# Kernel tuning notes

Measured on AMD Instinct MI355X. Metric: run time of the kernel, lower is better.

Reference implementation:

```python
import jax, jax.numpy as jnp
import numpy as np

EMBED_DIM = 1024
NUM_HEADS = 16
HEAD_DIM = EMBED_DIM // NUM_HEADS
B, S = 2, 2048


def setup_inputs() -> dict:
    key = jax.random.key(0)
    ks = jax.random.split(key, 10)
    inp = {
        "query": jax.random.normal(ks[0], (B, S, EMBED_DIM), dtype=jnp.float32),
        "key": jax.random.normal(ks[1], (B, S, EMBED_DIM), dtype=jnp.float32),
        "value": jax.random.normal(ks[2], (B, S, EMBED_DIM), dtype=jnp.float32),
        # 0 => masked key position (matches attn_mask == 0 in the torch code)
        "attn_mask": jax.random.randint(ks[3], (B, S), 0, 2, dtype=jnp.int32),
        "Wq": jax.random.normal(ks[4], (EMBED_DIM, EMBED_DIM), dtype=jnp.float32) * 0.02,
        "bq": jnp.zeros((EMBED_DIM,), dtype=jnp.float32),
        "Wk": jax.random.normal(ks[5], (EMBED_DIM, EMBED_DIM), dtype=jnp.float32) * 0.02,
        "bk": jnp.zeros((EMBED_DIM,), dtype=jnp.float32),
        "Wv": jax.random.normal(ks[6], (EMBED_DIM, EMBED_DIM), dtype=jnp.float32) * 0.02,
        "bv": jnp.zeros((EMBED_DIM,), dtype=jnp.float32),
    }
    return inp


def _proj_heads(x, W, b):
    # x: [B, S, E] -> [B, H, S, D]  (nn.Linear uses x @ W.T + b)
    y = x @ W.T + b
    Bx, Sx, E = y.shape
    return y.reshape(Bx, Sx, NUM_HEADS, HEAD_DIM).transpose(0, 2, 1, 3)


def reference(query, key, value, attn_mask, Wq, bq, Wk, bk, Wv, bv):
    q = _proj_heads(query, Wq, bq)   # [B,H,S,D]
    k = _proj_heads(key, Wk, bk)     # [B,H,S,D]
    v = _proj_heads(value, Wv, bv)   # [B,H,S,D]
    inv_scale = float(EMBED_DIM) ** 0.5  # NOTE: original divides by sqrt(embed_dim), not sqrt(head_dim)
    scores = jnp.einsum("bhqd,bhkd->bhqk", q, k) / inv_scale  # [B,H,S,S]
    mask = (attn_mask == 0)[:, None, None, :]  # [B,1,1,S] -> broadcast over [B,H,S,S]
    scores = jnp.where(mask, -jnp.inf, scores)
    attn = jax.nn.softmax(scores, axis=-1)
    # dropout omitted for deterministic reference (see notes)
    out = jnp.einsum("bhqk,bhkd->bhqd", attn, v)  # [B,H,S,D]
    return out
```

## Files before the change

kernel.cpp:

```cpp
#include <hip/hip_runtime.h>
#include <hip/hip_bf16.h>

constexpr int BB = 2;
constexpr int SS = 2048;
constexpr int EE = 1024;
constexpr int HH = 16;
constexpr int DD = 64;
constexpr int MM = BB * SS;
constexpr int CX = MM * EE;
constexpr int CW = EE * EE;
#define QSCALE 0.045084220027780106f
#define NEGBIG -1e30f

typedef __attribute__((ext_vector_type(8))) short short8;
typedef __attribute__((ext_vector_type(4))) float floatx4;

__device__ inline short bf16bits(float x) {
    __hip_bfloat16 h = __float2bfloat16(x);
    return *reinterpret_cast<short*>(&h);
}

__device__ inline unsigned pkbf(float a, float b) {
    return (unsigned)(unsigned short)bf16bits(a) |
           ((unsigned)(unsigned short)bf16bits(b) << 16);
}

__device__ inline float fast_exp2(float x) {
#if __has_builtin(__builtin_amdgcn_exp2f)
    return __builtin_amdgcn_exp2f(x);
#else
    return exp2f(x);
#endif
}

__device__ inline void gl_lds16(const __hip_bfloat16* g, short* l) {
    __builtin_amdgcn_global_load_lds(
        (const __attribute__((address_space(1))) void*)g,
        (__attribute__((address_space(3))) void*)l, 16, 0, 0);
}

__global__ __launch_bounds__(256) void convert_kernel(
    const float* __restrict__ x0, const float* __restrict__ x1, const float* __restrict__ x2,
    const float* __restrict__ w0, const float* __restrict__ w1, const float* __restrict__ w2,
    __hip_bfloat16* __restrict__ xb, __hip_bfloat16* __restrict__ wb)
{
    const int z = blockIdx.z;
    const float* src;
    __hip_bfloat16* dst;
    int count;
    if (z < 3) {
        src = (z == 0) ? x0 : (z == 1) ? x1 : x2;
        dst = xb + (size_t)z * CX;
        count = CX;
    } else {
        src = (z == 3) ? w0 : (z == 4) ? w1 : w2;
        dst = wb + (size_t)(z - 3) * CW;
        count = CW;
    }
    const int idx = (blockIdx.x * 256 + threadIdx.x) * 8;
    if (idx >= count) return;
    const float4 a = reinterpret_cast<const float4*>(src + idx)[0];
    const float4 b = reinterpret_cast<const float4*>(src + idx)[1];
    short8 r;
    r[0] = bf16bits(a.x); r[1] = bf16bits(a.y); r[2] = bf16bits(a.z); r[3] = bf16bits(a.w);
    r[4] = bf16bits(b.x); r[5] = bf16bits(b.y); r[6] = bf16bits(b.z); r[7] = bf16bits(b.w);
    *reinterpret_cast<short8*>(dst + idx) = r;
}

__global__ __launch_bounds__(256) void maskbias_kernel(
    const int* __restrict__ am, float* __restrict__ mb)
{
    const int i = blockIdx.x * 256 + threadIdx.x;
    if (i < BB * SS) mb[i] = (am[i] != 0) ? 0.f : NEGBIG;
}

__global__ __launch_bounds__(256) void proj_gemm(
    const __hip_bfloat16* __restrict__ xb,
    const __hip_bfloat16* __restrict__ wb,
    const float* __restrict__ bq, const float* __restrict__ bk, const float* __restrict__ bv,
    __hip_bfloat16* __restrict__ qws,
    __hip_bfloat16* __restrict__ kws,
    __hip_bfloat16* __restrict__ vtws)
{
    const int which = blockIdx.z;
    const __hip_bfloat16* A = xb + (size_t)which * CX;
    const __hip_bfloat16* W = wb + (size_t)which * CW;
    const float* bias = (which == 0) ? bq : (which == 1) ? bk : bv;

    const int m0   = blockIdx.x * 128;
    const int n0   = blockIdx.y * 128;
    const int tid  = threadIdx.x;
    const int wave = tid >> 6;
    const int lane = tid & 63;
    const int l15  = lane & 15;
    const int quad = lane >> 4;
    const int wr   = wave >> 1;
    const int wc   = wave & 1;

    __shared__ __align__(16) short As[128 * 32];
    __shared__ __align__(16) short Bs[128 * 32];

    const int lrow = (lane >> 2);
    const int lk   = (lane & 3) * 8;

    floatx4 acc[4][4] = {};

    for (int k0 = 0; k0 < EE; k0 += 32) {
        __syncthreads();
        #pragma unroll
        for (int i = 0; i < 2; ++i) {
            gl_lds16(A + (size_t)(m0 + i * 64 + wave * 16 + lrow) * EE + k0 + lk,
                     As + (i * 64 + wave * 16) * 32);
            gl_lds16(W + (size_t)(n0 + i * 64 + wave * 16 + lrow) * EE + k0 + lk,
                     Bs + (i * 64 + wave * 16) * 32);
        }
        __syncthreads();

        short8 af[4], bf[4];
        #pragma unroll
        for (int mt = 0; mt < 4; ++mt)
            af[mt] = *reinterpret_cast<const short8*>(As + (wr * 64 + mt * 16 + l15) * 32 + quad * 8);
        #pragma unroll
        for (int nt = 0; nt < 4; ++nt)
            bf[nt] = *reinterpret_cast<const short8*>(Bs + (wc * 64 + nt * 16 + l15) * 32 + quad * 8);

        #pragma unroll
        for (int mt = 0; mt < 4; ++mt)
            #pragma unroll
            for (int nt = 0; nt < 4; ++nt)
                acc[mt][nt] = __builtin_amdgcn_mfma_f32_16x16x32_bf16(af[mt], bf[nt], acc[mt][nt], 0, 0, 0);
    }

    #pragma unroll
    for (int nt = 0; nt < 4; ++nt) {
        const int n = n0 + wc * 64 + nt * 16 + l15;
        const float bval = bias[n];
        const int h = n >> 6, d = n & 63;
        #pragma unroll
        for (int mt = 0; mt < 4; ++mt) {
            #pragma unroll
            for (int r = 0; r < 4; ++r) {
                const int m = m0 + wr * 64 + mt * 16 + quad * 4 + r;
                const int b = m >> 11;
                const int s = m & (SS - 1);
                float val = acc[mt][nt][r] + bval;
                if (which == 0) val *= QSCALE;
                const __hip_bfloat16 hv = __float2bfloat16(val);
                if (which == 0)
                    qws[(((size_t)b * HH + h) * SS + s) * DD + d] = hv;
                else if (which == 1)
                    kws[(((size_t)b * HH + h) * SS + s) * DD + d] = hv;
                else
                    vtws[(((size_t)b * HH + h) * DD + d) * SS + s] = hv;
            }
        }
    }
}

__global__ __launch_bounds__(256) void attn_kernel(
    const __hip_bfloat16* __restrict__ qws,
    const __hip_bfloat16* __restrict__ kws,
    const __hip_bfloat16* __restrict__ vtws,
    const float* __restrict__ maskbias,
    float* __restrict__ out)
{
    const int bh   = blockIdx.y;
    const int b    = bh >> 4;
    const int q0   = blockIdx.x * 64;
    const int tid  = threadIdx.x;
    const int wave = tid >> 6;
    const int lane = tid & 63;
    const int l15  = lane & 15;
    const int quad = lane >> 4;

    const __hip_bfloat16* Q  = qws  + (size_t)bh * SS * DD;
    const __hip_bfloat16* K  = kws  + (size_t)bh * SS * DD;
    const __hip_bfloat16* VT = vtws + (size_t)bh * DD * SS;
    const float* mb = maskbias + b * SS;

    __shared__ __align__(16) short Ks[64 * 72];
    __shared__ __align__(16) short Vs[64 * 72];
    __shared__ __align__(16) short Ps[4][16 * 72];
    short* pw = Ps[wave];

    const int qrow = q0 + wave * 16 + l15;
    const short8 qa0 = *reinterpret_cast<const short8*>(Q + (size_t)qrow * DD + quad * 8);
    const short8 qa1 = *reinterpret_cast<const short8*>(Q + (size_t)qrow * DD + 32 + quad * 8);

    float m_run = NEGBIG, l_run = 0.f;
    floatx4 acc[4] = {};

    for (int kt = 0; kt < SS; kt += 64) {
        __syncthreads();

        #pragma unroll
        for (int p = 0; p < 2; ++p) {
            const int flat = tid + p * 256;
            const int row = flat >> 3;
            const int g   = flat & 7;
            *reinterpret_cast<short8*>(Ks + row * 72 + g * 8) =
                *reinterpret_cast<const short8*>(K + (size_t)(kt + row) * DD + g * 8);
            *reinterpret_cast<short8*>(Vs + row * 72 + g * 8) =
                *reinterpret_cast<const short8*>(VT + (size_t)row * SS + kt + g * 8);
        }
        __syncthreads();

        floatx4 st[4];
        #pragma unroll
        for (int f = 0; f < 4; ++f) {
            const short8 ka = *reinterpret_cast<const short8*>(Ks + (f * 16 + l15) * 72 + quad * 8);
            const short8 kb = *reinterpret_cast<const short8*>(Ks + (f * 16 + l15) * 72 + 32 + quad * 8);
            floatx4 z = {};
            z = __builtin_amdgcn_mfma_f32_16x16x32_bf16(ka, qa0, z, 0, 0, 0);
            z = __builtin_amdgcn_mfma_f32_16x16x32_bf16(kb, qa1, z, 0, 0, 0);
            st[f] = z;
        }

        #pragma unroll
        for (int f = 0; f < 4; ++f) {
            const float4 m4 = *reinterpret_cast<const float4*>(mb + kt + f * 16 + quad * 4);
            st[f][0] += m4.x; st[f][1] += m4.y; st[f][2] += m4.z; st[f][3] += m4.w;
        }

        float mx = st[0][0];
        #pragma unroll
        for (int f = 0; f < 4; ++f)
            #pragma unroll
            for (int r = 0; r < 4; ++r)
                mx = fmaxf(mx, st[f][r]);
        mx = fmaxf(mx, __shfl_xor(mx, 16, 64));
        mx = fmaxf(mx, __shfl_xor(mx, 32, 64));

        const float mnew = fmaxf(m_run, mx);
        const float alpha = fast_exp2(m_run - mnew);
        m_run = mnew;

        float psum = 0.f;
        #pragma unroll
        for (int f = 0; f < 4; ++f)
            #pragma unroll
            for (int r = 0; r < 4; ++r) {
                const float p = fast_exp2(st[f][r] - mnew);
                st[f][r] = p;
                psum += p;
            }
        psum += __shfl_xor(psum, 16, 64);
        psum += __shfl_xor(psum, 32, 64);
        l_run = l_run * alpha + psum;

        #pragma unroll
        for (int f = 0; f < 4; ++f) {
            *reinterpret_cast<unsigned*>(pw + l15 * 72 + f * 16 + quad * 4) =
                pkbf(st[f][0], st[f][1]);
            *reinterpret_cast<unsigned*>(pw + l15 * 72 + f * 16 + quad * 4 + 2) =
                pkbf(st[f][2], st[f][3]);
        }
        __asm__ volatile("s_waitcnt lgkmcnt(0)" ::: "memory");

        const short8 pa0 = *reinterpret_cast<const short8*>(pw + l15 * 72 + quad * 8);
        const short8 pa1 = *reinterpret_cast<const short8*>(pw + l15 * 72 + 32 + quad * 8);

        float alphaq[4];
        #pragma unroll
        for (int r = 0; r < 4; ++r)
            alphaq[r] = __shfl(alpha, quad * 4 + r, 16);
        #pragma unroll
        for (int nt = 0; nt < 4; ++nt)
            #pragma unroll
            for (int r = 0; r < 4; ++r)
                acc[nt][r] *= alphaq[r];

        #pragma unroll
        for (int nt = 0; nt < 4; ++nt) {
            const short8 vb0 = *reinterpret_cast<const short8*>(Vs + (nt * 16 + l15) * 72 + quad * 8);
            const short8 vb1 = *reinterpret_cast<const short8*>(Vs + (nt * 16 + l15) * 72 + 32 + quad * 8);
            acc[nt] = __builtin_amdgcn_mfma_f32_16x16x32_bf16(pa0, vb0, acc[nt], 0, 0, 0);
            acc[nt] = __builtin_amdgcn_mfma_f32_16x16x32_bf16(pa1, vb1, acc[nt], 0, 0, 0);
        }
    }

    float lq[4];
    #pragma unroll
    for (int r = 0; r < 4; ++r)
        lq[r] = __shfl(l_run, quad * 4 + r, 16);
    const size_t obase = (size_t)bh * SS * DD;
    #pragma unroll
    for (int nt = 0; nt < 4; ++nt)
        #pragma unroll
        for (int r = 0; r < 4; ++r) {
            const int qq = q0 + wave * 16 + quad * 4 + r;
            const int d  = nt * 16 + l15;
            out[obase + (size_t)qq * DD + d] = acc[nt][r] / lq[r];
        }
}

extern "C" void kernel_launch(void* const* d_in, const int* in_sizes, int n_in,
                              void* d_out, int out_size, void* d_ws, size_t ws_size,
                              hipStream_t stream) {
    const float* q    = (const float*)d_in[0];
    const float* k    = (const float*)d_in[1];
    const float* v    = (const float*)d_in[2];
    const int*   mask = (const int*)d_in[3];
    const float* Wq   = (const float*)d_in[4];
    const float* bq   = (const float*)d_in[5];
    const float* Wk   = (const float*)d_in[6];
    const float* bk   = (const float*)d_in[7];
    const float* Wv   = (const float*)d_in[8];
    const float* bv   = (const float*)d_in[9];
    float* out = (float*)d_out;

    __hip_bfloat16* qws  = (__hip_bfloat16*)d_ws;
    __hip_bfloat16* kws  = qws + (size_t)CX;
    __hip_bfloat16* vtws = kws + (size_t)CX;
    __hip_bfloat16* xb   = vtws + (size_t)CX;
    __hip_bfloat16* wb   = xb + (size_t)3 * CX;
    float* mbias = (float*)(wb + (size_t)3 * CW);

    convert_kernel<<<dim3(CX / (256 * 8), 1, 6), 256, 0, stream>>>(
        q, k, v, Wq, Wk, Wv, xb, wb);
    maskbias_kernel<<<dim3((BB * SS) / 256), 256, 0, stream>>>(mask, mbias);
    proj_gemm<<<dim3(MM / 128, EE / 128, 3), 256, 0, stream>>>(
        xb, wb, bq, bk, bv, qws, kws, vtws);
    attn_kernel<<<dim3(SS / 64, BB * HH), 256, 0, stream>>>(
        qws, kws, vtws, mbias, out);
}
```

Measured before the change: 235.3 us.

## Double-buffer LDS tiles with async global-to-LDS loads and XOR-swizzled layouts

The projection GEMM and the attention kernel now use double-buffered LDS tiles. The next K-tile is issued with global_load_lds before the current one is consumed, which lets each iteration drop to a single barrier and overlap global loads with MFMA work. The attention kernel also replaces its padded K/V/P layouts (stride 72) with unpadded rows and an XOR swizzle, so K and V can be DMA'd straight into LDS without bank conflicts. The convert kernel now runs on a flat 1D grid sized to the real element count instead of launching idle blocks for the smaller weight tensors. The cost is twice the LDS per block and a correctness dependence on the async loads being complete at the single barrier.

```diff
diff --git a/kernel.cpp b/kernel.cpp
--- a/kernel.cpp
+++ b/kernel.cpp
@@ -33,7 +33,7 @@
 #endif
 }
 
-__device__ inline void gl_lds16(const __hip_bfloat16* g, short* l) {
+__device__ inline void gl_lds16(const __hip_bfloat16* g, const short* l) {
     __builtin_amdgcn_global_load_lds(
         (const __attribute__((address_space(1))) void*)g,
         (__attribute__((address_space(3))) void*)l, 16, 0, 0);
@@ -44,27 +44,27 @@
     const float* __restrict__ w0, const float* __restrict__ w1, const float* __restrict__ w2,
     __hip_bfloat16* __restrict__ xb, __hip_bfloat16* __restrict__ wb)
 {
-    const int z = blockIdx.z;
+    const long long e = (long long)(blockIdx.x * 256 + threadIdx.x) * 8;
     const float* src;
     __hip_bfloat16* dst;
-    int count;
-    if (z < 3) {
-        src = (z == 0) ? x0 : (z == 1) ? x1 : x2;
-        dst = xb + (size_t)z * CX;
-        count = CX;
+    if (e < 3LL * CX) {
+        const int z = (int)(e >> 22);
+        const int off = (int)(e & (CX - 1));
+        src = ((z == 0) ? x0 : (z == 1) ? x1 : x2) + off;
+        dst = xb + e;
     } else {
-        src = (z == 3) ? w0 : (z == 4) ? w1 : w2;
-        dst = wb + (size_t)(z - 3) * CW;
-        count = CW;
+        const long long e2 = e - 3LL * CX;
+        const int z = (int)(e2 >> 20);
+        const int off = (int)(e2 & (CW - 1));
+        src = ((z == 0) ? w0 : (z == 1) ? w1 : w2) + off;
+        dst = wb + e2;
     }
-    const int idx = (blockIdx.x * 256 + threadIdx.x) * 8;
-    if (idx >= count) return;
-    const float4 a = reinterpret_cast<const float4*>(src + idx)[0];
-    const float4 b = reinterpret_cast<const float4*>(src + idx)[1];
+    const float4 a = reinterpret_cast<const float4*>(src)[0];
+    const float4 b = reinterpret_cast<const float4*>(src)[1];
     short8 r;
     r[0] = bf16bits(a.x); r[1] = bf16bits(a.y); r[2] = bf16bits(a.z); r[3] = bf16bits(a.w);
     r[4] = bf16bits(b.x); r[5] = bf16bits(b.y); r[6] = bf16bits(b.z); r[7] = bf16bits(b.w);
-    *reinterpret_cast<short8*>(dst + idx) = r;
+    *reinterpret_cast<short8*>(dst) = r;
 }
 
 __global__ __launch_bounds__(256) void maskbias_kernel(
@@ -97,32 +97,37 @@
     const int wr   = wave >> 1;
     const int wc   = wave & 1;
 
-    __shared__ __align__(16) short As[128 * 32];
-    __shared__ __align__(16) short Bs[128 * 32];
-
-    const int lrow = (lane >> 2);
+    __shared__ __align__(16) short As[2][128 * 32];
+    __shared__ __align__(16) short Bs[2][128 * 32];
+
+    const int lrow = lane >> 2;
     const int lk   = (lane & 3) * 8;
 
     floatx4 acc[4][4] = {};
 
-    for (int k0 = 0; k0 < EE; k0 += 32) {
+    auto issue = [&](int k0, int buf) {
+        #pragma unroll
+        for (int i = 0; i < 2; ++i) {
+            const int row = i * 64 + wave * 16;
+            gl_lds16(A + (size_t)(m0 + row + lrow) * EE + k0 + lk, &As[buf][row * 32]);
+            gl_lds16(W + (size_t)(n0 + row + lrow) * EE + k0 + lk, &Bs[buf][row * 32]);
+        }
+    };
+
+    issue(0, 0);
+
+    for (int t = 0; t < EE / 32; ++t) {
+        const int buf = t & 1;
         __syncthreads();
-        #pragma unroll
-        for (int i = 0; i < 2; ++i) {
-            gl_lds16(A + (size_t)(m0 + i * 64 + wave * 16 + lrow) * EE + k0 + lk,
-                     As + (i * 64 + wave * 16) * 32);
-            gl_lds16(W + (size_t)(n0 + i * 64 + wave * 16 + lrow) * EE + k0 + lk,
-                     Bs + (i * 64 + wave * 16) * 32);
-        }
-        __syncthreads();
+        if (t + 1 < EE / 32) issue((t + 1) * 32, buf ^ 1);
 
         short8 af[4], bf[4];
         #pragma unroll
         for (int mt = 0; mt < 4; ++mt)
-            af[mt] = *reinterpret_cast<const short8*>(As + (wr * 64 + mt * 16 + l15) * 32 + quad * 8);
+            af[mt] = *reinterpret_cast<const short8*>(&As[buf][(wr * 64 + mt * 16 + l15) * 32 + quad * 8]);
         #pragma unroll
         for (int nt = 0; nt < 4; ++nt)
-            bf[nt] = *reinterpret_cast<const short8*>(Bs + (wc * 64 + nt * 16 + l15) * 32 + quad * 8);
+            bf[nt] = *reinterpret_cast<const short8*>(&Bs[buf][(wc * 64 + nt * 16 + l15) * 32 + quad * 8]);
 
         #pragma unroll
         for (int mt = 0; mt < 4; ++mt)
@@ -178,38 +183,46 @@
     const __hip_bfloat16* VT = vtws + (size_t)bh * DD * SS;
     const float* mb = maskbias + b * SS;
 
-    __shared__ __align__(16) short Ks[64 * 72];
-    __shared__ __align__(16) short Vs[64 * 72];
-    __shared__ __align__(16) short Ps[4][16 * 72];
+    __shared__ __align__(16) short Ks[2][64 * 64];
+    __shared__ __align__(16) short Vs[2][64 * 64];
+    __shared__ __align__(16) short Ps[4][16 * 64];
     short* pw = Ps[wave];
 
     const int qrow = q0 + wave * 16 + l15;
     const short8 qa0 = *reinterpret_cast<const short8*>(Q + (size_t)qrow * DD + quad * 8);
     const short8 qa1 = *reinterpret_cast<const short8*>(Q + (size_t)qrow * DD + 32 + quad * 8);
 
+    const int srow = lane >> 3;
+    const int sg   = ((lane & 7) ^ srow) * 8;
+
+    auto issue = [&](int kt, int buf) {
+        #pragma unroll
+        for (int p = 0; p < 2; ++p) {
+            const int rb = wave * 16 + p * 8;
+            gl_lds16(K + (size_t)(kt + rb + srow) * DD + sg, &Ks[buf][rb * 64]);
+            gl_lds16(VT + (size_t)(rb + srow) * SS + kt + sg, &Vs[buf][rb * 64]);
+        }
+    };
+
+    const int swz = (l15 & 7);
+
     float m_run = NEGBIG, l_run = 0.f;
     floatx4 acc[4] = {};
 
-    for (int kt = 0; kt < SS; kt += 64) {
+    issue(0, 0);
+
+    for (int t = 0; t < SS / 64; ++t) {
+        const int buf = t & 1;
+        const int kt = t * 64;
         __syncthreads();
-
-        #pragma unroll
-        for (int p = 0; p < 2; ++p) {
-            const int flat = tid + p * 256;
-            const int row = flat >> 3;
-            const int g   = flat & 7;
-            *reinterpret_cast<short8*>(Ks + row * 72 + g * 8) =
-                *reinterpret_cast<const short8*>(K + (size_t)(kt + row) * DD + g * 8);
-            *reinterpret_cast<short8*>(Vs + row * 72 + g * 8) =
-                *reinterpret_cast<const short8*>(VT + (size_t)row * SS + kt + g * 8);
-        }
-        __syncthreads();
+        if (t + 1 < SS / 64) issue(kt + 64, buf ^ 1);
 
         floatx4 st[4];
         #pragma unroll
         for (int f = 0; f < 4; ++f) {
-            const short8 ka = *reinterpret_cast<const short8*>(Ks + (f * 16 + l15) * 72 + quad * 8);
-            const short8 kb = *reinterpret_cast<const short8*>(Ks + (f * 16 + l15) * 72 + 32 + quad * 8);
+            const int krow = (f * 16 + l15) * 64;
+            const short8 ka = *reinterpret_cast<const short8*>(&Ks[buf][krow + (quad ^ swz) * 8]);
+            const short8 kb = *reinterpret_cast<const short8*>(&Ks[buf][krow + ((quad + 4) ^ swz) * 8]);
             floatx4 z = {};
             z = __builtin_amdgcn_mfma_f32_16x16x32_bf16(ka, qa0, z, 0, 0, 0);
             z = __builtin_amdgcn_mfma_f32_16x16x32_bf16(kb, qa1, z, 0, 0, 0);
@@ -250,15 +263,16 @@
 
         #pragma unroll
         for (int f = 0; f < 4; ++f) {
-            *reinterpret_cast<unsigned*>(pw + l15 * 72 + f * 16 + quad * 4) =
-                pkbf(st[f][0], st[f][1]);
-            *reinterpret_cast<unsigned*>(pw + l15 * 72 + f * 16 + quad * 4 + 2) =
-                pkbf(st[f][2], st[f][3]);
+            const int g0 = (2 * f + (quad >> 1)) ^ swz;
+            uint2 pk;
+            pk.x = pkbf(st[f][0], st[f][1]);
+            pk.y = pkbf(st[f][2], st[f][3]);
+            *reinterpret_cast<uint2*>(pw + l15 * 64 + g0 * 8 + (quad & 1) * 4) = pk;
         }
         __asm__ volatile("s_waitcnt lgkmcnt(0)" ::: "memory");
 
-        const short8 pa0 = *reinterpret_cast<const short8*>(pw + l15 * 72 + quad * 8);
-        const short8 pa1 = *reinterpret_cast<const short8*>(pw + l15 * 72 + 32 + quad * 8);
+        const short8 pa0 = *reinterpret_cast<const short8*>(pw + l15 * 64 + (quad ^ swz) * 8);
+        const short8 pa1 = *reinterpret_cast<const short8*>(pw + l15 * 64 + ((quad + 4) ^ swz) * 8);
 
         float alphaq[4];
         #pragma unroll
@@ -272,8 +286,9 @@
 
         #pragma unroll
         for (int nt = 0; nt < 4; ++nt) {
-            const short8 vb0 = *reinterpret_cast<const short8*>(Vs + (nt * 16 + l15) * 72 + quad * 8);
-            const short8 vb1 = *reinterpret_cast<const short8*>(Vs + (nt * 16 + l15) * 72 + 32 + quad * 8);
+            const int vrow = (nt * 16 + l15) * 64;
+            const short8 vb0 = *reinterpret_cast<const short8*>(&Vs[buf][vrow + (quad ^ swz) * 8]);
+            const short8 vb1 = *reinterpret_cast<const short8*>(&Vs[buf][vrow + ((quad + 4) ^ swz) * 8]);
             acc[nt] = __builtin_amdgcn_mfma_f32_16x16x32_bf16(pa0, vb0, acc[nt], 0, 0, 0);
             acc[nt] = __builtin_amdgcn_mfma_f32_16x16x32_bf16(pa1, vb1, acc[nt], 0, 0, 0);
         }
@@ -316,8 +331,8 @@
     __hip_bfloat16* wb   = xb + (size_t)3 * CX;
     float* mbias = (float*)(wb + (size_t)3 * CW);
 
-    convert_kernel<<<dim3(CX / (256 * 8), 1, 6), 256, 0, stream>>>(
-        q, k, v, Wq, Wk, Wv, xb, wb);
+    const int cvt_blocks = (3 * CX + 3 * CW) / (256 * 8);
+    convert_kernel<<<dim3(cvt_blocks), 256, 0, stream>>>(q, k, v, Wq, Wk, Wv, xb, wb);
     maskbias_kernel<<<dim3((BB * SS) / 256), 256, 0, stream>>>(mask, mbias);
     proj_gemm<<<dim3(MM / 128, EE / 128, 3), 256, 0, stream>>>(
         xb, wb, bq, bk, bv, qws, kws, vtws);
```

Result: slower. 251.8 us (+7.0%).
